# Kernel tuning notes

Hardware: AMD Instinct MI355X
Metric: run time of the kernel (lower is better)

The kernel has to match this reference:

```python
import jax, jax.numpy as jnp
import numpy as np

B, S, H = 2, 2048, 1024          # batch, seq, hidden_size
I = 512                          # expert_ffn_hidden_size
E_R, E_Z = 32, 8                 # routed experts, zero (identity) experts
E_T = E_R + E_Z                  # total experts
K = 6                            # moe_topk
SCALE = 2.5                      # routed_scaling_factor
W_INIT = 0.02


def setup_inputs() -> dict:
    key = jax.random.key(0)
    k0, k1, k2, k3 = jax.random.split(key, 4)
    return {
        "hidden_states": jax.random.normal(k0, (B, S, H), jnp.float32),
        "classifier_weight": jax.random.normal(k1, (E_T, H), jnp.float32) * W_INIT,
        "e_score_correction_bias": jnp.zeros((E_T,), jnp.float32),
        "gate_up_proj": jax.random.normal(k2, (E_T, 2 * I, H), jnp.float32) * W_INIT,
        "down_proj": jax.random.normal(k3, (E_R, H, I), jnp.float32) * W_INIT,
    }


def reference(hidden_states, classifier_weight, e_score_correction_bias,
              gate_up_proj, down_proj):
    orig_shape = hidden_states.shape
    x = hidden_states.reshape(-1, H).astype(jnp.float32)      # [T, H]
    T = x.shape[0]

    # ---- router (fp32 like the torch code) ----
    logits = x @ classifier_weight.T                          # [T, E_T]
    scores = jax.nn.softmax(logits, axis=-1)
    _, topk_idx = jax.lax.top_k(scores + e_score_correction_bias[None, :], K)
    topk_w = jnp.take_along_axis(scores, topk_idx, axis=1) * SCALE  # [T, K]

    # dense per-(token, expert) combine weights; 0 for unselected experts
    w_full = jnp.zeros((T, E_T), jnp.float32).at[
        jnp.arange(T)[:, None], topk_idx].add(topk_w)          # [T, E_T]

    # zero experts: weighted identity
    zero_w = w_full[:, E_R:].sum(axis=-1, keepdims=True)       # [T, 1]
    out0 = x * zero_w

    # routed experts: SwiGLU MLP per expert, scanned over experts
    routed_w = w_full[:, :E_R].T                               # [E_R, T]

    def body(out, xs):
        Wgu, Wd, we = xs                                       # [2I,H],[H,I],[T]
        gate, up = jnp.split(x @ Wgu.T, 2, axis=-1)            # [T, I] each
        y = (jax.nn.silu(gate) * up) @ Wd.T                    # [T, H]
        return out + we[:, None] * y, None

    out, _ = jax.lax.scan(body, out0, (gate_up_proj[:E_R], down_proj, routed_w))
    return out.reshape(orig_shape).astype(hidden_states.dtype)
```

## Files before the change

kernel.cpp:

```cpp
#include <hip/hip_runtime.h>
#include <float.h>
#include <math.h>

#define TT 4096
#define HH 1024
#define II 512
#define E_R 32
#define E_T 40
#define TOPK 6
#define SCALE_F 2.5f
#define MAXTILES 224

typedef __bf16 bf16x8 __attribute__((ext_vector_type(8)));
typedef float f32x4 __attribute__((ext_vector_type(4)));

__device__ inline unsigned short f2bf(float f) {
  __bf16 h = (__bf16)f;
  return __builtin_bit_cast(unsigned short, h);
}

__device__ inline uint4 cvt8(float4 a, float4 b) {
  bf16x8 v;
  v[0] = (__bf16)a.x; v[1] = (__bf16)a.y; v[2] = (__bf16)a.z; v[3] = (__bf16)a.w;
  v[4] = (__bf16)b.x; v[5] = (__bf16)b.y; v[6] = (__bf16)b.z; v[7] = (__bf16)b.w;
  return __builtin_bit_cast(uint4, v);
}

__device__ inline void gload_lds16(const void* g, void* l) {
  __builtin_amdgcn_global_load_lds(
      (__attribute__((address_space(1))) void*)g,
      (__attribute__((address_space(3))) void*)l, 16, 0, 0);
}

__device__ inline void lds_store16(unsigned short* base, int row, int c8, uint4 v) {
  int byte = (row * 128 + c8 * 16) ^ ((row & 7) << 4);
  *reinterpret_cast<uint4*>(reinterpret_cast<char*>(base) + byte) = v;
}
__device__ inline bf16x8 lds_frag(const unsigned short* base, int row, int kb) {
  int byte = (row * 128 + kb * 2) ^ ((row & 7) << 4);
  uint4 v = *reinterpret_cast<const uint4*>(reinterpret_cast<const char*>(base) + byte);
  return __builtin_bit_cast(bf16x8, v);
}

__device__ inline f32x4 mfma16(bf16x8 a, bf16x8 b, f32x4 c) {
  return __builtin_amdgcn_mfma_f32_16x16x32_bf16(a, b, c, 0, 0, 0);
}

__global__ void k_convert_x(const float* __restrict__ x, unsigned short* __restrict__ xb) {
  int i = blockIdx.x * 256 + threadIdx.x;
  const float4* p = reinterpret_cast<const float4*>(x) + (size_t)i * 2;
  float4 a = p[0], b = p[1];
  reinterpret_cast<uint4*>(xb)[i] = cvt8(a, b);
}

__global__ __launch_bounds__(256) void k_logits(const float* __restrict__ x,
                                                const float* __restrict__ wcls,
                                                float* __restrict__ logits) {
  __shared__ float4 ws4[E_T * 64];
  const int tid = threadIdx.x;
  const int lane = tid & 63;
  const int wave = tid >> 6;
  const int token = blockIdx.x * 4 + wave;
  const float4* x4 = reinterpret_cast<const float4*>(x);
  const float4* w4 = reinterpret_cast<const float4*>(wcls);

  float acc[E_T];
  #pragma unroll
  for (int e = 0; e < E_T; ++e) acc[e] = 0.f;

  for (int c = 0; c < 4; ++c) {
    if (c) __syncthreads();
    #pragma unroll
    for (int j = 0; j < 10; ++j) {
      int v = tid + j * 256;
      int e = v >> 6, kq = v & 63;
      ws4[v] = w4[e * 256 + c * 64 + kq];
    }
    float4 xv = x4[(size_t)token * 256 + c * 64 + lane];
    __syncthreads();
    #pragma unroll
    for (int e = 0; e < E_T; ++e) {
      float4 w = ws4[e * 64 + lane];
      acc[e] += xv.x * w.x + xv.y * w.y + xv.z * w.z + xv.w * w.w;
    }
  }

  float mine = 0.f;
  #pragma unroll
  for (int e = 0; e < E_T; ++e) {
    float r = acc[e];
    #pragma unroll
    for (int o = 32; o; o >>= 1) r += __shfl_xor(r, o);
    if (lane == e) mine = r;
  }
  if (lane < E_T) logits[(size_t)token * E_T + lane] = mine;
}

__global__ void k_topk(const float* __restrict__ logits, const float* __restrict__ bias,
                       float* __restrict__ zero_w, int* __restrict__ counts,
                       int* __restrict__ tok_list,
                       int* __restrict__ route_ep, float* __restrict__ route_w,
                       int* __restrict__ route_n) {
  int t = blockIdx.x * 64 + threadIdx.x;
  float l[E_T];
  const float4* lp = reinterpret_cast<const float4*>(logits + (size_t)t * E_T);
  #pragma unroll
  for (int j = 0; j < E_T / 4; ++j) {
    float4 v = lp[j];
    l[j * 4 + 0] = v.x; l[j * 4 + 1] = v.y; l[j * 4 + 2] = v.z; l[j * 4 + 3] = v.w;
  }
  float m = -FLT_MAX;
  #pragma unroll
  for (int e = 0; e < E_T; ++e) m = fmaxf(m, l[e]);
  float den = 0.f;
  #pragma unroll
  for (int e = 0; e < E_T; ++e) { l[e] = __expf(l[e] - m); den += l[e]; }
  float inv = 1.f / den;
  float sel[E_T];
  #pragma unroll
  for (int e = 0; e < E_T; ++e) { l[e] *= inv; sel[e] = l[e] + bias[e]; }

  unsigned long long used = 0ull;
  float zw = 0.f;
  int nr = 0;
  for (int k = 0; k < TOPK; ++k) {
    float bv = -FLT_MAX; int bj = 0;
    #pragma unroll
    for (int e = 0; e < E_T; ++e) {
      float v = ((used >> e) & 1ull) ? -FLT_MAX : sel[e];
      if (v > bv) { bv = v; bj = e; }
    }
    used |= 1ull << bj;
    float wgt = (bv - bias[bj]) * SCALE_F;
    if (bj >= E_R) {
      zw += wgt;
    } else {
      int p = atomicAdd(&counts[bj], 1);
      tok_list[bj * TT + p] = t;
      route_ep[t * TOPK + nr] = (bj << 16) | p;
      route_w[t * TOPK + nr] = wgt;
      nr++;
    }
  }
  zero_w[t] = zw;
  route_n[t] = nr;
}

__global__ void k_scan(const int* __restrict__ counts, int* __restrict__ offsets,
                       int* __restrict__ tiles) {
  if (threadIdx.x == 0) {
    int s = 0, idx = 0;
    for (int e = 0; e < E_R; ++e) {
      offsets[e] = s;
      int c = counts[e];
      s += c;
      for (int r0 = 0; r0 < c; r0 += 128) tiles[1 + idx++] = (e << 16) | r0;
    }
    offsets[E_R] = s;
    tiles[0] = idx;
  }
}

__global__ __launch_bounds__(256, 3) void k_gemm1(
    const unsigned short* __restrict__ xb, const float* __restrict__ gup,
    const int* __restrict__ tok_list, const int* __restrict__ counts,
    const int* __restrict__ offsets, const int* __restrict__ tiles,
    unsigned short* __restrict__ inter) {
  const int nt = tiles[0];
  if ((int)blockIdx.y >= nt) return;
  const int tv = tiles[1 + blockIdx.y];
  const int e = tv >> 16;
  const int row0 = tv & 0xffff;
  const int cnt = counts[e];
  const int off = offsets[e];
  const int n0 = blockIdx.x * 64;
  const int tid = threadIdx.x;
  const int lane = tid & 63;
  const int wave = tid >> 6;
  const int wr = wave >> 1;
  const int wc = wave & 1;

  __shared__ __align__(16) unsigned short lA[128 * 64];
  __shared__ __align__(16) unsigned short lBg[64 * 64];
  __shared__ __align__(16) unsigned short lBu[64 * 64];
  __shared__ int toks[128];

  if (tid < 128) {
    int r = row0 + tid;
    toks[tid] = tok_list[e * TT + (r < cnt ? r : cnt - 1)];
  }
  __syncthreads();

  size_t asrc[4];
  #pragma unroll
  for (int i = 0; i < 4; ++i) {
    int lrow = wave * 32 + i * 8 + (lane >> 3);
    asrc[i] = (size_t)toks[lrow] * HH + (((lane & 7) ^ (lrow & 7)) * 8);
  }
  int brow[2], bc8[2];
  const float4* bgp[2]; const float4* bup[2];
  #pragma unroll
  for (int s = 0; s < 2; ++s) {
    int idx = tid + s * 256;
    brow[s] = idx >> 3; bc8[s] = idx & 7;
    bgp[s] = reinterpret_cast<const float4*>(
        gup + ((size_t)e * 1024 + n0 + brow[s]) * HH) + bc8[s] * 2;
    bup[s] = reinterpret_cast<const float4*>(
        gup + ((size_t)e * 1024 + 512 + n0 + brow[s]) * HH) + bc8[s] * 2;
  }

  f32x4 accg[4][2] = {}; f32x4 accu[4][2] = {};

  for (int k0 = 0; k0 < HH; k0 += 64) {
    int kq = k0 >> 2;
    #pragma unroll
    for (int i = 0; i < 4; ++i)
      gload_lds16(xb + asrc[i] + k0, lA + (wave * 32 + i * 8) * 64);
    #pragma unroll
    for (int s = 0; s < 2; ++s) {
      float4 ga = bgp[s][kq], gb = bgp[s][kq + 1];
      lds_store16(lBg, brow[s], bc8[s], cvt8(ga, gb));
      float4 ua = bup[s][kq], ub = bup[s][kq + 1];
      lds_store16(lBu, brow[s], bc8[s], cvt8(ua, ub));
    }
    __syncthreads();
    #pragma unroll
    for (int ks = 0; ks < 2; ++ks) {
      int kb = ks * 32 + ((lane >> 4) << 3);
      bf16x8 a[4], g[2], u[2];
      #pragma unroll
      for (int i = 0; i < 4; ++i) a[i] = lds_frag(lA, wr * 64 + i * 16 + (lane & 15), kb);
      #pragma unroll
      for (int j = 0; j < 2; ++j) {
        g[j] = lds_frag(lBg, wc * 32 + j * 16 + (lane & 15), kb);
        u[j] = lds_frag(lBu, wc * 32 + j * 16 + (lane & 15), kb);
      }
      #pragma unroll
      for (int i = 0; i < 4; ++i)
        #pragma unroll
        for (int j = 0; j < 2; ++j) {
          accg[i][j] = mfma16(a[i], g[j], accg[i][j]);
          accu[i][j] = mfma16(a[i], u[j], accu[i][j]);
        }
    }
    __syncthreads();
  }

  #pragma unroll
  for (int i = 0; i < 4; ++i)
    #pragma unroll
    for (int j = 0; j < 2; ++j)
      #pragma unroll
      for (int r = 0; r < 4; ++r) {
        int rloc = wr * 64 + i * 16 + ((lane >> 4) << 2) + r;
        int grow = row0 + rloc;
        if (grow < cnt) {
          int col = n0 + wc * 32 + j * 16 + (lane & 15);
          float gv = accg[i][j][r], uv = accu[i][j][r];
          float act = gv / (1.f + __expf(-gv)) * uv;
          inter[(size_t)(off + grow) * II + col] = f2bf(act);
        }
      }
}

__global__ __launch_bounds__(256, 3) void k_gemm2(
    const unsigned short* __restrict__ inter, const float* __restrict__ dwn,
    const int* __restrict__ counts, const int* __restrict__ offsets,
    const int* __restrict__ tiles, unsigned short* __restrict__ inter2) {
  const int nt = tiles[0];
  if ((int)blockIdx.y >= nt) return;
  const int tv = tiles[1 + blockIdx.y];
  const int e = tv >> 16;
  const int row0 = tv & 0xffff;
  const int cnt = counts[e];
  const int off = offsets[e];
  const int h0 = blockIdx.x * 128;
  const int tid = threadIdx.x;
  const int lane = tid & 63;
  const int wave = tid >> 6;
  const int wr = wave >> 1;
  const int wc = wave & 1;

  __shared__ __align__(16) unsigned short lA[128 * 64];
  __shared__ __align__(16) unsigned short lB[128 * 64];

  size_t asrc[4];
  #pragma unroll
  for (int i = 0; i < 4; ++i) {
    int lrow = wave * 32 + i * 8 + (lane >> 3);
    int rr = row0 + lrow; rr = rr < cnt ? rr : cnt - 1;
    asrc[i] = (size_t)(off + rr) * II + (((lane & 7) ^ (lrow & 7)) * 8);
  }
  int brow[4], bc8[4];
  const float4* bp[4];
  #pragma unroll
  for (int s = 0; s < 4; ++s) {
    int idx = tid + s * 256;
    brow[s] = idx >> 3; bc8[s] = idx & 7;
    bp[s] = reinterpret_cast<const float4*>(
        dwn + ((size_t)e * HH + h0 + brow[s]) * II) + bc8[s] * 2;
  }

  f32x4 acc[4][4] = {};

  for (int k0 = 0; k0 < II; k0 += 64) {
    int kq = k0 >> 2;
    #pragma unroll
    for (int i = 0; i < 4; ++i)
      gload_lds16(inter + asrc[i] + k0, lA + (wave * 32 + i * 8) * 64);
    #pragma unroll
    for (int s = 0; s < 4; ++s) {
      float4 a = bp[s][kq], b = bp[s][kq + 1];
      lds_store16(lB, brow[s], bc8[s], cvt8(a, b));
    }
    __syncthreads();
    #pragma unroll
    for (int ks = 0; ks < 2; ++ks) {
      int kb = ks * 32 + ((lane >> 4) << 3);
      bf16x8 a[4], b[4];
      #pragma unroll
      for (int i = 0; i < 4; ++i) a[i] = lds_frag(lA, wr * 64 + i * 16 + (lane & 15), kb);
      #pragma unroll
      for (int j = 0; j < 4; ++j) b[j] = lds_frag(lB, wc * 64 + j * 16 + (lane & 15), kb);
      #pragma unroll
      for (int i = 0; i < 4; ++i)
        #pragma unroll
        for (int j = 0; j < 4; ++j)
          acc[i][j] = mfma16(a[i], b[j], acc[i][j]);
    }
    __syncthreads();
  }

  #pragma unroll
  for (int i = 0; i < 4; ++i)
    #pragma unroll
    for (int j = 0; j < 4; ++j)
      #pragma unroll
      for (int r = 0; r < 4; ++r) {
        int rloc = wr * 64 + i * 16 + ((lane >> 4) << 2) + r;
        int grow = row0 + rloc;
        if (grow < cnt) {
          int h = h0 + wc * 64 + j * 16 + (lane & 15);
          inter2[(size_t)(off + grow) * HH + h] = f2bf(acc[i][j][r]);
        }
      }
}

__global__ __launch_bounds__(256) void k_combine(
    const float* __restrict__ x, const float* __restrict__ zero_w,
    const int* __restrict__ offsets, const int* __restrict__ route_ep,
    const float* __restrict__ route_w, const int* __restrict__ route_n,
    const unsigned short* __restrict__ inter2, float* __restrict__ out) {
  const int t = blockIdx.x;
  const int tid = threadIdx.x;
  const float zw = zero_w[t];
  const int n = route_n[t];
  float4 o = reinterpret_cast<const float4*>(x)[t * 256 + tid];
  o.x *= zw; o.y *= zw; o.z *= zw; o.w *= zw;
  for (int i = 0; i < n; ++i) {
    int ep = route_ep[t * TOPK + i];
    int row = offsets[ep >> 16] + (ep & 0xffff);
    float w = route_w[t * TOPK + i];
    ushort4 v = reinterpret_cast<const ushort4*>(inter2 + (size_t)row * HH)[tid];
    o.x += w * __builtin_bit_cast(float, (unsigned)v.x << 16);
    o.y += w * __builtin_bit_cast(float, (unsigned)v.y << 16);
    o.z += w * __builtin_bit_cast(float, (unsigned)v.z << 16);
    o.w += w * __builtin_bit_cast(float, (unsigned)v.w << 16);
  }
  reinterpret_cast<float4*>(out)[t * 256 + tid] = o;
}


extern "C" void kernel_launch(void* const* d_in, const int* in_sizes, int n_in,
                              void* d_out, int out_size, void* d_ws, size_t ws_size,
                              hipStream_t stream) {
  const float* x    = (const float*)d_in[0];
  const float* wcls = (const float*)d_in[1];
  const float* bias = (const float*)d_in[2];
  const float* gup  = (const float*)d_in[3];
  const float* dwn  = (const float*)d_in[4];
  float* out = (float*)d_out;

  char* w = (char*)d_ws;
  unsigned short* xb    = (unsigned short*)(w + 0);
  float* zero_w         = (float*)(w + 8388608);
  int* counts           = (int*)(w + 8404992);
  int* offsets          = (int*)(w + 8405120);
  int* tok_list         = (int*)(w + 8405376);
  float* logits         = (float*)(w + 8929664);
  int* tiles            = (int*)(w + 9585024);
  int* route_ep         = (int*)(w + 9589120);
  float* route_w        = (float*)(w + 9687424);
  int* route_n          = (int*)(w + 9785728);
  unsigned short* inter = (unsigned short*)(w + 9802112);
  unsigned short* inter2 = (unsigned short*)(w + 34967936);

  hipMemsetAsync(counts, 0, E_R * sizeof(int), stream);
  k_convert_x<<<2048, 256, 0, stream>>>(x, xb);
  k_logits<<<1024, 256, 0, stream>>>(x, wcls, logits);
  k_topk<<<64, 64, 0, stream>>>(logits, bias, zero_w, counts, tok_list,
                                route_ep, route_w, route_n);
  k_scan<<<1, 64, 0, stream>>>(counts, offsets, tiles);
  k_gemm1<<<dim3(8, MAXTILES), 256, 0, stream>>>(xb, gup, tok_list, counts, offsets, tiles, inter);
  k_gemm2<<<dim3(8, MAXTILES), 256, 0, stream>>>(inter, dwn, counts, offsets, tiles, inter2);
  k_combine<<<TT, 256, 0, stream>>>(x, zero_w, offsets, route_ep, route_w, route_n,
                                    inter2, out);
}
```

Measured before the change: 231.1 us.

## Double-buffer LDS tiles in expert GEMMs and fuse x bf16 conversion into router

Both expert GEMM kernels now use ping-pong LDS buffers. The next K-slice's global loads are issued before the current slice's MFMAs, and the converted weights are written to LDS afterwards, so memory latency overlaps with compute and one barrier per iteration is removed. Launch bounds drop from 3 to 2 blocks per CU to fit the doubled shared memory, which lowers occupancy. Separately, the standalone x-to-bf16 conversion kernel is removed, and the router logits kernel now writes the bf16 copy of x as it reads x.

```diff
diff --git a/kernel.cpp b/kernel.cpp
--- a/kernel.cpp
+++ b/kernel.cpp
@@ -46,16 +46,10 @@
   return __builtin_amdgcn_mfma_f32_16x16x32_bf16(a, b, c, 0, 0, 0);
 }
 
-__global__ void k_convert_x(const float* __restrict__ x, unsigned short* __restrict__ xb) {
-  int i = blockIdx.x * 256 + threadIdx.x;
-  const float4* p = reinterpret_cast<const float4*>(x) + (size_t)i * 2;
-  float4 a = p[0], b = p[1];
-  reinterpret_cast<uint4*>(xb)[i] = cvt8(a, b);
-}
-
 __global__ __launch_bounds__(256) void k_logits(const float* __restrict__ x,
                                                 const float* __restrict__ wcls,
-                                                float* __restrict__ logits) {
+                                                float* __restrict__ logits,
+                                                unsigned short* __restrict__ xb) {
   __shared__ float4 ws4[E_T * 64];
   const int tid = threadIdx.x;
   const int lane = tid & 63;
@@ -77,6 +71,9 @@
       ws4[v] = w4[e * 256 + c * 64 + kq];
     }
     float4 xv = x4[(size_t)token * 256 + c * 64 + lane];
+    ushort4 s;
+    s.x = f2bf(xv.x); s.y = f2bf(xv.y); s.z = f2bf(xv.z); s.w = f2bf(xv.w);
+    reinterpret_cast<ushort4*>(xb + (size_t)token * HH)[c * 64 + lane] = s;
     __syncthreads();
     #pragma unroll
     for (int e = 0; e < E_T; ++e) {
@@ -161,7 +158,7 @@
   }
 }
 
-__global__ __launch_bounds__(256, 3) void k_gemm1(
+__global__ __launch_bounds__(256, 2) void k_gemm1(
     const unsigned short* __restrict__ xb, const float* __restrict__ gup,
     const int* __restrict__ tok_list, const int* __restrict__ counts,
     const int* __restrict__ offsets, const int* __restrict__ tiles,
@@ -180,9 +177,9 @@
   const int wr = wave >> 1;
   const int wc = wave & 1;
 
-  __shared__ __align__(16) unsigned short lA[128 * 64];
-  __shared__ __align__(16) unsigned short lBg[64 * 64];
-  __shared__ __align__(16) unsigned short lBu[64 * 64];
+  __shared__ __align__(16) unsigned short lA0[128 * 64], lA1[128 * 64];
+  __shared__ __align__(16) unsigned short lBg0[64 * 64], lBg1[64 * 64];
+  __shared__ __align__(16) unsigned short lBu0[64 * 64], lBu1[64 * 64];
   __shared__ int toks[128];
 
   if (tid < 128) {
@@ -211,29 +208,50 @@
 
   f32x4 accg[4][2] = {}; f32x4 accu[4][2] = {};
 
-  for (int k0 = 0; k0 < HH; k0 += 64) {
-    int kq = k0 >> 2;
-    #pragma unroll
-    for (int i = 0; i < 4; ++i)
-      gload_lds16(xb + asrc[i] + k0, lA + (wave * 32 + i * 8) * 64);
-    #pragma unroll
-    for (int s = 0; s < 2; ++s) {
-      float4 ga = bgp[s][kq], gb = bgp[s][kq + 1];
-      lds_store16(lBg, brow[s], bc8[s], cvt8(ga, gb));
-      float4 ua = bup[s][kq], ub = bup[s][kq + 1];
-      lds_store16(lBu, brow[s], bc8[s], cvt8(ua, ub));
-    }
-    __syncthreads();
+  #pragma unroll
+  for (int i = 0; i < 4; ++i)
+    gload_lds16(xb + asrc[i], lA0 + (wave * 32 + i * 8) * 64);
+  #pragma unroll
+  for (int s = 0; s < 2; ++s) {
+    float4 ga = bgp[s][0], gb = bgp[s][1];
+    lds_store16(lBg0, brow[s], bc8[s], cvt8(ga, gb));
+    float4 ua = bup[s][0], ub = bup[s][1];
+    lds_store16(lBu0, brow[s], bc8[s], cvt8(ua, ub));
+  }
+  __syncthreads();
+
+  for (int t = 0; t < 16; ++t) {
+    const bool last = (t == 15);
+    unsigned short* cA  = (t & 1) ? lA1 : lA0;
+    unsigned short* cBg = (t & 1) ? lBg1 : lBg0;
+    unsigned short* cBu = (t & 1) ? lBu1 : lBu0;
+    unsigned short* nA  = (t & 1) ? lA0 : lA1;
+    unsigned short* nBg = (t & 1) ? lBg0 : lBg1;
+    unsigned short* nBu = (t & 1) ? lBu0 : lBu1;
+
+    float4 ga[2], gb[2], ua[2], ub[2];
+    if (!last) {
+      int k1 = (t + 1) * 64, kq = k1 >> 2;
+      #pragma unroll
+      for (int i = 0; i < 4; ++i)
+        gload_lds16(xb + asrc[i] + k1, nA + (wave * 32 + i * 8) * 64);
+      #pragma unroll
+      for (int s = 0; s < 2; ++s) {
+        ga[s] = bgp[s][kq]; gb[s] = bgp[s][kq + 1];
+        ua[s] = bup[s][kq]; ub[s] = bup[s][kq + 1];
+      }
+    }
+
     #pragma unroll
     for (int ks = 0; ks < 2; ++ks) {
       int kb = ks * 32 + ((lane >> 4) << 3);
       bf16x8 a[4], g[2], u[2];
       #pragma unroll
-      for (int i = 0; i < 4; ++i) a[i] = lds_frag(lA, wr * 64 + i * 16 + (lane & 15), kb);
+      for (int i = 0; i < 4; ++i) a[i] = lds_frag(cA, wr * 64 + i * 16 + (lane & 15), kb);
       #pragma unroll
       for (int j = 0; j < 2; ++j) {
-        g[j] = lds_frag(lBg, wc * 32 + j * 16 + (lane & 15), kb);
-        u[j] = lds_frag(lBu, wc * 32 + j * 16 + (lane & 15), kb);
+        g[j] = lds_frag(cBg, wc * 32 + j * 16 + (lane & 15), kb);
+        u[j] = lds_frag(cBu, wc * 32 + j * 16 + (lane & 15), kb);
       }
       #pragma unroll
       for (int i = 0; i < 4; ++i)
@@ -242,6 +260,14 @@
           accg[i][j] = mfma16(a[i], g[j], accg[i][j]);
           accu[i][j] = mfma16(a[i], u[j], accu[i][j]);
         }
+    }
+
+    if (!last) {
+      #pragma unroll
+      for (int s = 0; s < 2; ++s) {
+        lds_store16(nBg, brow[s], bc8[s], cvt8(ga[s], gb[s]));
+        lds_store16(nBu, brow[s], bc8[s], cvt8(ua[s], ub[s]));
+      }
     }
     __syncthreads();
   }
@@ -263,7 +289,7 @@
       }
 }
 
-__global__ __launch_bounds__(256, 3) void k_gemm2(
+__global__ __launch_bounds__(256, 2) void k_gemm2(
     const unsigned short* __restrict__ inter, const float* __restrict__ dwn,
     const int* __restrict__ counts, const int* __restrict__ offsets,
     const int* __restrict__ tiles, unsigned short* __restrict__ inter2) {
@@ -281,8 +307,8 @@
   const int wr = wave >> 1;
   const int wc = wave & 1;
 
-  __shared__ __align__(16) unsigned short lA[128 * 64];
-  __shared__ __align__(16) unsigned short lB[128 * 64];
+  __shared__ __align__(16) unsigned short lA0[128 * 64], lA1[128 * 64];
+  __shared__ __align__(16) unsigned short lB0[128 * 64], lB1[128 * 64];
 
   size_t asrc[4];
   #pragma unroll
@@ -303,30 +329,52 @@
 
   f32x4 acc[4][4] = {};
 
-  for (int k0 = 0; k0 < II; k0 += 64) {
-    int kq = k0 >> 2;
-    #pragma unroll
-    for (int i = 0; i < 4; ++i)
-      gload_lds16(inter + asrc[i] + k0, lA + (wave * 32 + i * 8) * 64);
-    #pragma unroll
-    for (int s = 0; s < 4; ++s) {
-      float4 a = bp[s][kq], b = bp[s][kq + 1];
-      lds_store16(lB, brow[s], bc8[s], cvt8(a, b));
-    }
-    __syncthreads();
+  #pragma unroll
+  for (int i = 0; i < 4; ++i)
+    gload_lds16(inter + asrc[i], lA0 + (wave * 32 + i * 8) * 64);
+  #pragma unroll
+  for (int s = 0; s < 4; ++s) {
+    float4 a = bp[s][0], b = bp[s][1];
+    lds_store16(lB0, brow[s], bc8[s], cvt8(a, b));
+  }
+  __syncthreads();
+
+  for (int t = 0; t < 8; ++t) {
+    const bool last = (t == 7);
+    unsigned short* cA = (t & 1) ? lA1 : lA0;
+    unsigned short* cB = (t & 1) ? lB1 : lB0;
+    unsigned short* nA = (t & 1) ? lA0 : lA1;
+    unsigned short* nB = (t & 1) ? lB0 : lB1;
+
+    float4 pa[4], pb[4];
+    if (!last) {
+      int k1 = (t + 1) * 64, kq = k1 >> 2;
+      #pragma unroll
+      for (int i = 0; i < 4; ++i)
+        gload_lds16(inter + asrc[i] + k1, nA + (wave * 32 + i * 8) * 64);
+      #pragma unroll
+      for (int s = 0; s < 4; ++s) { pa[s] = bp[s][kq]; pb[s] = bp[s][kq + 1]; }
+    }
+
     #pragma unroll
     for (int ks = 0; ks < 2; ++ks) {
       int kb = ks * 32 + ((lane >> 4) << 3);
       bf16x8 a[4], b[4];
       #pragma unroll
-      for (int i = 0; i < 4; ++i) a[i] = lds_frag(lA, wr * 64 + i * 16 + (lane & 15), kb);
-      #pragma unroll
-      for (int j = 0; j < 4; ++j) b[j] = lds_frag(lB, wc * 64 + j * 16 + (lane & 15), kb);
+      for (int i = 0; i < 4; ++i) a[i] = lds_frag(cA, wr * 64 + i * 16 + (lane & 15), kb);
+      #pragma unroll
+      for (int j = 0; j < 4; ++j) b[j] = lds_frag(cB, wc * 64 + j * 16 + (lane & 15), kb);
       #pragma unroll
       for (int i = 0; i < 4; ++i)
         #pragma unroll
         for (int j = 0; j < 4; ++j)
           acc[i][j] = mfma16(a[i], b[j], acc[i][j]);
+    }
+
+    if (!last) {
+      #pragma unroll
+      for (int s = 0; s < 4; ++s)
+        lds_store16(nB, brow[s], bc8[s], cvt8(pa[s], pb[s]));
     }
     __syncthreads();
   }
@@ -396,8 +444,7 @@
   unsigned short* inter2 = (unsigned short*)(w + 34967936);
 
   hipMemsetAsync(counts, 0, E_R * sizeof(int), stream);
-  k_convert_x<<<2048, 256, 0, stream>>>(x, xb);
-  k_logits<<<1024, 256, 0, stream>>>(x, wcls, logits);
+  k_logits<<<1024, 256, 0, stream>>>(x, wcls, logits, xb);
   k_topk<<<64, 64, 0, stream>>>(logits, bias, zero_w, counts, tok_list,
                                 route_ep, route_w, route_n);
   k_scan<<<1, 64, 0, stream>>>(counts, offsets, tiles);
```

Result: slower. 271.7 us (+17.6%).
